# Kernel optimization log

Hardware: AMD Instinct MI355X
Metric: run time of the kernel (lower is better)

## Reference

```python
import jax, jax.numpy as jnp
import numpy as np

D_MODEL, D_STATE, D_INNER, DT_RANK, K = 64, 16, 128, 4, 4
EPS = 1e-6  # RMSNorm eps


def setup_inputs() -> dict:
    key = jax.random.key(0)
    ks = jax.random.split(key, 12)
    B, L = 8, 4096
    s = 0.02
    x = jax.random.normal(ks[0], (B, L, D_MODEL), dtype=jnp.float32)
    w_norm = jnp.ones((D_MODEL,), jnp.float32)
    W_in = jax.random.normal(ks[1], (2 * D_INNER, D_MODEL), jnp.float32) * s
    b_in = jnp.zeros((2 * D_INNER,), jnp.float32)
    W_conv = jax.random.normal(ks[2], (D_INNER, D_INNER, K), jnp.float32) * s
    b_conv = jnp.zeros((D_INNER,), jnp.float32)
    W_xp = jax.random.normal(ks[3], (DT_RANK + 2 * D_STATE, D_INNER), jnp.float32) * s
    b_xp = jnp.zeros((DT_RANK + 2 * D_STATE,), jnp.float32)
    W_dt = jax.random.normal(ks[4], (D_INNER, DT_RANK), jnp.float32) * s
    b_dt = jnp.zeros((D_INNER,), jnp.float32)
    W_out = jax.random.normal(ks[5], (D_MODEL, D_INNER), jnp.float32) * s
    b_out = jnp.zeros((D_MODEL,), jnp.float32)
    A_log = jnp.log(jnp.tile(jnp.arange(1, D_STATE + 1, dtype=jnp.float32), (D_INNER, 1)))
    D_param = jnp.ones((D_INNER,), jnp.float32)
    return dict(x=x, w_norm=w_norm, W_in=W_in, b_in=b_in, W_conv=W_conv, b_conv=b_conv,
                W_xp=W_xp, b_xp=b_xp, W_dt=W_dt, b_dt=b_dt, W_out=W_out, b_out=b_out,
                A_log=A_log, D_param=D_param)


def _mamba_block(xn, W_in, b_in, W_conv, b_conv, W_xp, b_xp, W_dt, b_dt, W_out, b_out, A_log, D_param):
    B, L, _ = xn.shape
    xz = xn @ W_in.T + b_in                      # (B,L,2*d_inner)
    u, z = jnp.split(xz, 2, axis=-1)
    z = jax.nn.silu(z)
    # conv1d: NCH, causal-style pad (K-1) both sides then truncate to L
    uc = jax.lax.conv_general_dilated(
        u.transpose(0, 2, 1), W_conv, window_strides=(1,), padding=[(K - 1, K - 1)],
        dimension_numbers=("NCH", "OIH", "NCH"))[:, :, :L] + b_conv[None, :, None]
    u = jax.nn.silu(uc.transpose(0, 2, 1))       # (B,L,d_inner)
    xp = u @ W_xp.T + b_xp
    dt, Bm, Cm = jnp.split(xp, [DT_RANK, DT_RANK + D_STATE], axis=-1)
    delta = jax.nn.softplus(dt @ W_dt.T + b_dt)  # (B,L,d_inner)
    A = -jnp.exp(A_log)                          # (d_inner, n)
    A_bar = jnp.exp(jnp.einsum('bld,dn->bldn', delta, A))
    B_bar_x = jnp.einsum('bld,bln,bld->bldn', delta, Bm, u)

    def step(h, inp):
        a, bx, c = inp                           # (B,d,n),(B,d,n),(B,n)
        h = a * h + bx
        y = jnp.einsum('bdn,bn->bd', h, c)
        return h, y

    h0 = jnp.zeros((B, D_INNER, D_STATE), xn.dtype)
    xs = (A_bar.transpose(1, 0, 2, 3), B_bar_x.transpose(1, 0, 2, 3), Cm.transpose(1, 0, 2))
    _, ys = jax.lax.scan(step, h0, xs)           # (L,B,d_inner)
    y = ys.transpose(1, 0, 2) + D_param * u
    y = y * z
    return y @ W_out.T + b_out


def reference(x, w_norm, W_in, b_in, W_conv, b_conv, W_xp, b_xp, W_dt, b_dt, W_out, b_out, A_log, D_param):
    xn = x * jax.lax.rsqrt(jnp.mean(x * x, axis=-1, keepdims=True) + EPS) * w_norm
    return x + _mamba_block(xn, W_in, b_in, W_conv, b_conv, W_xp, b_xp, W_dt, b_dt, W_out, b_out, A_log, D_param)
```

## Files before the change

### kernel.cpp

```cpp
#include <hip/hip_runtime.h>
#include <math.h>

#define D_MODEL 64
#define D_STATE 16
#define D_INNER 128
#define DT_RANK 4
#define BB 8
#define LL 4096
#define NTOK (BB*LL)
#define EPSV 1e-6f
#define NCHUNK 64
#define LC (LL/NCHUNK)
#define PAD 136
#define PADF 132

typedef __attribute__((ext_vector_type(8))) short bf16x8;
typedef __attribute__((ext_vector_type(4))) float f32x4;

__device__ __forceinline__ float sig_(float v) { return 1.f / (1.f + __expf(-v)); }
__device__ __forceinline__ float softplus_(float v) {
    return (v > 20.f) ? v : __logf(1.f + __expf(v));
}
__device__ __forceinline__ unsigned short f2bf(float x) {
    unsigned int u = __float_as_uint(x);
    u += 0x7fff + ((u >> 16) & 1);
    return (unsigned short)(u >> 16);
}
__device__ __forceinline__ float bf2f(unsigned short u) {
    return __uint_as_float(((unsigned int)u) << 16);
}

__global__ __launch_bounds__(256) void pack_all(
    const float* __restrict__ W_in, const float* __restrict__ w_norm,
    const float* __restrict__ W_conv, const float* __restrict__ W_xp,
    const float* __restrict__ W_out,
    unsigned short* __restrict__ Win_bf, unsigned short* __restrict__ Bp,
    unsigned short* __restrict__ Wxp_bf, unsigned short* __restrict__ Wout_bf)
{
    int i = blockIdx.x * 256 + threadIdx.x;
    if (i < 16384) {
        Win_bf[i] = f2bf(W_in[i] * w_norm[i & 63]);
    } else if (i < 81920) {
        int j = i - 16384;
        int kk = j >> 14, o = (j >> 7) & 127, c = j & 127;
        Bp[j] = f2bf(W_conv[o * 512 + c * 4 + kk]);
    } else if (i < 88064) {
        int j = i - 81920;
        Wxp_bf[j] = ((j >> 7) < 36) ? f2bf(W_xp[j]) : (unsigned short)0;
    } else if (i < 96256) {
        int j = i - 88064;
        Wout_bf[j] = f2bf(W_out[j]);
    }
}

__global__ __launch_bounds__(256) void k1_fused(
    const float* __restrict__ x, const unsigned short* __restrict__ Win_bf,
    const float* __restrict__ b_in,
    unsigned short* __restrict__ u_bf, unsigned short* __restrict__ z_bf)
{
    __shared__ unsigned short axs[64 * 72];
    int tid = threadIdx.x;
    int tb = blockIdx.x * 64;
    {
        int t = tid >> 2, qt = tid & 3;
        float4 v[4];
        float ss = 0.f;
        #pragma unroll
        for (int j = 0; j < 4; ++j) {
            v[j] = *(const float4*)&x[(tb + t) * 64 + qt * 16 + j * 4];
            ss += v[j].x*v[j].x + v[j].y*v[j].y + v[j].z*v[j].z + v[j].w*v[j].w;
        }
        ss += __shfl_xor(ss, 1, 64);
        ss += __shfl_xor(ss, 2, 64);
        float r = rsqrtf(ss * (1.f / 64.f) + EPSV);
        unsigned short tmp[16];
        #pragma unroll
        for (int j = 0; j < 4; ++j) {
            tmp[4*j+0] = f2bf(v[j].x * r); tmp[4*j+1] = f2bf(v[j].y * r);
            tmp[4*j+2] = f2bf(v[j].z * r); tmp[4*j+3] = f2bf(v[j].w * r);
        }
        *(bf16x8*)&axs[t * 72 + qt * 16]     = *(bf16x8*)&tmp[0];
        *(bf16x8*)&axs[t * 72 + qt * 16 + 8] = *(bf16x8*)&tmp[8];
    }
    __syncthreads();
    int wave = tid >> 6, lane = tid & 63;
    int quad = lane >> 4, l16 = lane & 15;
    f32x4 acc[16];
    #pragma unroll
    for (int nt = 0; nt < 16; ++nt) acc[nt] = (f32x4){0.f, 0.f, 0.f, 0.f};
    bf16x8 a0 = *(const bf16x8*)&axs[(wave * 16 + l16) * 72 + quad * 8];
    bf16x8 a1 = *(const bf16x8*)&axs[(wave * 16 + l16) * 72 + 32 + quad * 8];
    #pragma unroll
    for (int nt = 0; nt < 16; ++nt) {
        bf16x8 b0 = *(const bf16x8*)&Win_bf[(nt * 16 + l16) * 64 + quad * 8];
        bf16x8 b1 = *(const bf16x8*)&Win_bf[(nt * 16 + l16) * 64 + 32 + quad * 8];
        acc[nt] = __builtin_amdgcn_mfma_f32_16x16x32_bf16(a0, b0, acc[nt], 0, 0, 0);
        acc[nt] = __builtin_amdgcn_mfma_f32_16x16x32_bf16(a1, b1, acc[nt], 0, 0, 0);
    }
    #pragma unroll
    for (int nt = 0; nt < 16; ++nt) {
        int o = nt * 16 + l16;
        float bo = b_in[o];
        #pragma unroll
        for (int r = 0; r < 4; ++r) {
            int t = tb + wave * 16 + quad * 4 + r;
            float v = acc[nt][r] + bo;
            if (o < 128) u_bf[t * 128 + o] = f2bf(v);
            else         z_bf[t * 128 + (o - 128)] = f2bf(v * sig_(v));
        }
    }
}

__global__ __launch_bounds__(256) void k2k3a_fused(
    const unsigned short* __restrict__ u_bf, const unsigned short* __restrict__ Bp,
    const float* __restrict__ b_conv,
    const unsigned short* __restrict__ Wxp_bf, const float* __restrict__ b_xp,
    const float* __restrict__ W_dt, const float* __restrict__ b_dt,
    const float* __restrict__ A_log,
    unsigned short* __restrict__ u_cbf, float* __restrict__ delta,
    float* __restrict__ Bm, float* __restrict__ Cm,
    float* __restrict__ P, float* __restrict__ Q)
{
    __shared__ unsigned short uls[64 * PAD];
    __shared__ float dls[64 * PADF];
    __shared__ float bls[64 * 16];
    __shared__ float dts[64][4];
    __shared__ float Wd[512];
    __shared__ float bds[128];
    int tid = threadIdx.x;
    if (tid < 128) *(float4*)&Wd[tid * 4] = *(const float4*)&W_dt[tid * 4];
    else if (tid < 160) *(float4*)&bds[(tid - 128) * 4] = *(const float4*)&b_dt[(tid - 128) * 4];
    int wave = tid >> 6, lane = tid & 63;
    int quad = lane >> 4, l16 = lane & 15;
    int tb = blockIdx.x * 64;
    int bbase = tb & ~4095;
    int t0 = tb + wave * 16;
    f32x4 acc[8];
    #pragma unroll
    for (int og = 0; og < 8; ++og) acc[og] = (f32x4){0.f, 0.f, 0.f, 0.f};
    int row_base = t0 + l16 - 3;
    #pragma unroll
    for (int kk = 0; kk < 4; ++kk) {
        int row = row_base + kk;
        #pragma unroll
        for (int cs = 0; cs < 4; ++cs) {
            int kbase = cs * 32 + quad * 8;
            bf16x8 a = {0,0,0,0,0,0,0,0};
            if (row >= bbase)
                a = *(const bf16x8*)&u_bf[row * 128 + kbase];
            #pragma unroll
            for (int og = 0; og < 8; ++og) {
                bf16x8 b = *(const bf16x8*)&Bp[kk * 16384 + (og * 16 + l16) * 128 + kbase];
                acc[og] = __builtin_amdgcn_mfma_f32_16x16x32_bf16(a, b, acc[og], 0, 0, 0);
            }
        }
    }
    #pragma unroll
    for (int og = 0; og < 8; ++og) {
        int o = og * 16 + l16;
        float bc = b_conv[o];
        #pragma unroll
        for (int r = 0; r < 4; ++r) {
            int tloc = wave * 16 + quad * 4 + r;
            float v = acc[og][r] + bc;
            unsigned short ub = f2bf(v * sig_(v));
            u_cbf[(tb + tloc) * 128 + o] = ub;
            uls[tloc * PAD + o] = ub;
        }
    }
    __syncthreads();
    f32x4 xacc[3];
    #pragma unroll
    for (int nt = 0; nt < 3; ++nt) xacc[nt] = (f32x4){0.f, 0.f, 0.f, 0.f};
    #pragma unroll
    for (int cs = 0; cs < 4; ++cs) {
        int kbase = cs * 32 + quad * 8;
        bf16x8 a = *(const bf16x8*)&uls[(wave * 16 + l16) * PAD + kbase];
        #pragma unroll
        for (int nt = 0; nt < 3; ++nt) {
            bf16x8 b = *(const bf16x8*)&Wxp_bf[(nt * 16 + l16) * 128 + kbase];
            xacc[nt] = __builtin_amdgcn_mfma_f32_16x16x32_bf16(a, b, xacc[nt], 0, 0, 0);
        }
    }
    #pragma unroll
    for (int nt = 0; nt < 3; ++nt) {
        int j = nt * 16 + l16;
        float bx = (j < 36) ? b_xp[j] : 0.f;
        #pragma unroll
        for (int r = 0; r < 4; ++r) {
            int tloc = wave * 16 + quad * 4 + r;
            int t = tb + tloc;
            float val = xacc[nt][r] + bx;
            if (j < 4) {
                dts[tloc][j] = val;
            } else if (j < 20) {
                Bm[t * 16 + (j - 4)] = val;
                bls[tloc * 16 + (j - 4)] = val;
            } else if (j < 36) {
                Cm[t * 16 + (j - 20)] = val;
            }
        }
    }
    __syncthreads();
    {
        int tokloc = tid >> 2, dgrp = tid & 3;
        float dt0 = dts[tokloc][0], dt1 = dts[tokloc][1],
              dt2 = dts[tokloc][2], dt3 = dts[tokloc][3];
        int g = tb + tokloc;
        #pragma unroll
        for (int d4 = 0; d4 < 8; ++d4) {
            int d = dgrp * 32 + d4 * 4;
            float4 w0 = *(const float4*)&Wd[(d + 0) * 4];
            float4 w1 = *(const float4*)&Wd[(d + 1) * 4];
            float4 w2 = *(const float4*)&Wd[(d + 2) * 4];
            float4 w3 = *(const float4*)&Wd[(d + 3) * 4];
            float4 bdv = *(const float4*)&bds[d];
            float4 r;
            r.x = softplus_(bdv.x + dt0*w0.x + dt1*w0.y + dt2*w0.z + dt3*w0.w);
            r.y = softplus_(bdv.y + dt0*w1.x + dt1*w1.y + dt2*w1.z + dt3*w1.w);
            r.z = softplus_(bdv.z + dt0*w2.x + dt1*w2.y + dt2*w2.z + dt3*w2.w);
            r.w = softplus_(bdv.w + dt0*w3.x + dt1*w3.y + dt2*w3.z + dt3*w3.w);
            *(float4*)&delta[g * 128 + d] = r;
            *(float4*)&dls[tokloc * PADF + d] = r;
        }
    }
    __syncthreads();
    {
        int d = tid >> 1;
        int nb = (tid & 1) * 8;
        float4 Av0 = *(const float4*)&A_log[d * 16 + nb];
        float4 Av1 = *(const float4*)&A_log[d * 16 + nb + 4];
        float A0 = -__expf(Av0.x), A1 = -__expf(Av0.y),
              A2 = -__expf(Av0.z), A3 = -__expf(Av0.w);
        float A4 = -__expf(Av1.x), A5 = -__expf(Av1.y),
              A6 = -__expf(Av1.z), A7 = -__expf(Av1.w);
        float P0=1.f,P1=1.f,P2=1.f,P3=1.f,P4=1.f,P5=1.f,P6=1.f,P7=1.f;
        float Q0=0.f,Q1=0.f,Q2=0.f,Q3=0.f,Q4=0.f,Q5=0.f,Q6=0.f,Q7=0.f;
        for (int t = 0; t < LC; ++t) {
            float dl = dls[t * PADF + d];
            float uu = bf2f(uls[t * PAD + d]);
            float4 bm0 = *(const float4*)&bls[t * 16 + nb];
            float4 bm1 = *(const float4*)&bls[t * 16 + nb + 4];
            float du = dl * uu;
            float a0 = __expf(dl * A0), a1 = __expf(dl * A1),
                  a2 = __expf(dl * A2), a3 = __expf(dl * A3);
            float a4 = __expf(dl * A4), a5 = __expf(dl * A5),
                  a6 = __expf(dl * A6), a7 = __expf(dl * A7);
            P0 *= a0; P1 *= a1; P2 *= a2; P3 *= a3;
            P4 *= a4; P5 *= a5; P6 *= a6; P7 *= a7;
            Q0 = a0 * Q0 + du * bm0.x; Q1 = a1 * Q1 + du * bm0.y;
            Q2 = a2 * Q2 + du * bm0.z; Q3 = a3 * Q3 + du * bm0.w;
            Q4 = a4 * Q4 + du * bm1.x; Q5 = a5 * Q5 + du * bm1.y;
            Q6 = a6 * Q6 + du * bm1.z; Q7 = a7 * Q7 + du * bm1.w;
        }
        int idx = blockIdx.x * 2048 + d * 16 + nb;
        *(float4*)&P[idx]     = (float4){P0, P1, P2, P3};
        *(float4*)&P[idx + 4] = (float4){P4, P5, P6, P7};
        *(float4*)&Q[idx]     = (float4){Q0, Q1, Q2, Q3};
        *(float4*)&Q[idx + 4] = (float4){Q4, Q5, Q6, Q7};
    }
}

__global__ __launch_bounds__(256) void k4b_carry(
    const float* __restrict__ P, const float* __restrict__ Q, float* __restrict__ Hinit)
{
    int tid = blockIdx.x * 256 + threadIdx.x;
    int b = tid >> 11, dn = tid & 2047;
    float carry = 0.f;
    for (int c = 0; c < NCHUNK; ++c) {
        int idx = (b * NCHUNK + c) * 2048 + dn;
        Hinit[idx] = carry;
        carry = P[idx] * carry + Q[idx];
    }
}

__global__ __launch_bounds__(256) void k4c_scan(
    const float* __restrict__ delta, const unsigned short* __restrict__ u_cbf,
    const float* __restrict__ Bm, const float* __restrict__ Cm,
    const unsigned short* __restrict__ z_bf, const float* __restrict__ A_log,
    const float* __restrict__ D_param, const float* __restrict__ Hinit,
    unsigned short* __restrict__ y_bf)
{
    __shared__ float dls[LC * 64];
    __shared__ unsigned short uls[LC * 64];
    __shared__ float bls[LC * 16];
    __shared__ float cls[LC * 16];
    __shared__ unsigned short zls[LC * 64];
    int bid = blockIdx.x;
    int b = bid >> 7, c = (bid >> 1) & 63, half = bid & 1;
    int tid = threadIdx.x, lane = tid & 63;
    int g0 = b * LL + c * LC;
    int d0 = half * 64;
    for (int i = tid; i < LC * 16; i += 256) {
        int row = i >> 4, q = i & 15;
        *(float4*)&dls[row * 64 + q * 4] =
            *(const float4*)&delta[(g0 + row) * 128 + d0 + q * 4];
    }
    for (int i = tid; i < LC * 8; i += 256) {
        int row = i >> 3, q = i & 7;
        *(float4*)&uls[row * 64 + q * 8] =
            *(const float4*)&u_cbf[(g0 + row) * 128 + d0 + q * 8];
        *(float4*)&zls[row * 64 + q * 8] =
            *(const float4*)&z_bf[(g0 + row) * 128 + d0 + q * 8];
    }
    for (int i = tid; i < LC * 4; i += 256) {
        int row = i >> 2, q = i & 3;
        *(float4*)&bls[row * 16 + q * 4] =
            *(const float4*)&Bm[(g0 + row) * 16 + q * 4];
        *(float4*)&cls[row * 16 + q * 4] =
            *(const float4*)&Cm[(g0 + row) * 16 + q * 4];
    }
    int dloc = (tid >> 6) * 16 + (lane >> 2);
    int d = d0 + dloc;
    int ng = lane & 3;
    float4 Av = *(const float4*)&A_log[d * 16 + ng * 4];
    float A0 = -__expf(Av.x), A1 = -__expf(Av.y), A2 = -__expf(Av.z), A3 = -__expf(Av.w);
    float4 h = *(const float4*)&Hinit[(b * NCHUNK + c) * 2048 + d * 16 + ng * 4];
    float Dp = D_param[d];
    __syncthreads();
    for (int t = 0; t < LC; ++t) {
        float dl = dls[t * 64 + dloc];
        float uu = bf2f(uls[t * 64 + dloc]);
        float4 bm = *(const float4*)&bls[t * 16 + ng * 4];
        float4 cm = *(const float4*)&cls[t * 16 + ng * 4];
        float du = dl * uu;
        float a0 = __expf(dl * A0), a1 = __expf(dl * A1),
              a2 = __expf(dl * A2), a3 = __expf(dl * A3);
        h.x = a0 * h.x + du * bm.x; h.y = a1 * h.y + du * bm.y;
        h.z = a2 * h.z + du * bm.z; h.w = a3 * h.w + du * bm.w;
        float yv = h.x * cm.x + h.y * cm.y + h.z * cm.z + h.w * cm.w;
        yv += __shfl_xor(yv, 1, 64);
        yv += __shfl_xor(yv, 2, 64);
        if (ng == 0) {
            float y = yv + Dp * uu;
            y *= bf2f(zls[t * 64 + dloc]);
            y_bf[(g0 + t) * 128 + d] = f2bf(y);
        }
    }
}

__global__ __launch_bounds__(256) void k5_outproj_mfma(
    const unsigned short* __restrict__ y_bf, const unsigned short* __restrict__ Wout_bf,
    const float* __restrict__ b_out, const float* __restrict__ x,
    float* __restrict__ out)
{
    int tid = threadIdx.x;
    int wave = tid >> 6, lane = tid & 63;
    int quad = lane >> 4, l16 = lane & 15;
    int t0 = blockIdx.x * 64 + wave * 16;
    f32x4 acc[4];
    #pragma unroll
    for (int nt = 0; nt < 4; ++nt) acc[nt] = (f32x4){0.f, 0.f, 0.f, 0.f};
    #pragma unroll
    for (int cs = 0; cs < 4; ++cs) {
        int kbase = cs * 32 + quad * 8;
        bf16x8 a = *(const bf16x8*)&y_bf[(t0 + l16) * 128 + kbase];
        #pragma unroll
        for (int nt = 0; nt < 4; ++nt) {
            bf16x8 b = *(const bf16x8*)&Wout_bf[(nt * 16 + l16) * 128 + kbase];
            acc[nt] = __builtin_amdgcn_mfma_f32_16x16x32_bf16(a, b, acc[nt], 0, 0, 0);
        }
    }
    #pragma unroll
    for (int nt = 0; nt < 4; ++nt) {
        int m = nt * 16 + l16;
        float bo = b_out[m];
        #pragma unroll
        for (int r = 0; r < 4; ++r) {
            int t = t0 + quad * 4 + r;
            out[t * 64 + m] = acc[nt][r] + bo + x[t * 64 + m];
        }
    }
}

extern "C" void kernel_launch(void* const* d_in, const int* in_sizes, int n_in,
                              void* d_out, int out_size, void* d_ws, size_t ws_size,
                              hipStream_t stream)
{
    const float* x       = (const float*)d_in[0];
    const float* w_norm  = (const float*)d_in[1];
    const float* W_in    = (const float*)d_in[2];
    const float* b_in    = (const float*)d_in[3];
    const float* W_conv  = (const float*)d_in[4];
    const float* b_conv  = (const float*)d_in[5];
    const float* W_xp    = (const float*)d_in[6];
    const float* b_xp    = (const float*)d_in[7];
    const float* W_dt    = (const float*)d_in[8];
    const float* b_dt    = (const float*)d_in[9];
    const float* W_out   = (const float*)d_in[10];
    const float* b_out   = (const float*)d_in[11];
    const float* A_log   = (const float*)d_in[12];
    const float* D_param = (const float*)d_in[13];
    float* ws = (float*)d_ws;

    unsigned short* u_bf = (unsigned short*)ws;
    unsigned short* y_bf = (unsigned short*)ws;
    unsigned short* z_bf = (unsigned short*)(ws + 2097152);
    unsigned short* u_cbf= (unsigned short*)(ws + 4194304);
    float* delta  = ws + 6291456;
    float* Bm     = ws + 10485760;
    float* Cm     = ws + 11010048;
    float* P      = ws + 11534336;
    float* Q      = ws + 12582912;
    float* Hinit  = ws + 13631488;
    unsigned short* Bp      = (unsigned short*)(ws + 14680064);
    unsigned short* Wxp_bf  = (unsigned short*)(ws + 14712832);
    unsigned short* Wout_bf = (unsigned short*)(ws + 14715904);
    unsigned short* Win_bf  = (unsigned short*)(ws + 14720000);
    float* out    = (float*)d_out;

    pack_all<<<376, 256, 0, stream>>>(W_in, w_norm, W_conv, W_xp, W_out,
                                      Win_bf, Bp, Wxp_bf, Wout_bf);
    k1_fused<<<512, 256, 0, stream>>>(x, Win_bf, b_in, u_bf, z_bf);
    k2k3a_fused<<<512, 256, 0, stream>>>(u_bf, Bp, b_conv, Wxp_bf, b_xp,
                                         W_dt, b_dt, A_log,
                                         u_cbf, delta, Bm, Cm, P, Q);
    k4b_carry<<<64, 256, 0, stream>>>(P, Q, Hinit);
    k4c_scan<<<1024, 256, 0, stream>>>(delta, u_cbf, Bm, Cm, z_bf, A_log,
                                       D_param, Hinit, y_bf);
    k5_outproj_mfma<<<512, 256, 0, stream>>>(y_bf, Wout_bf, b_out, x, out);
}
```

Before: 196.9 us.

## Fuse chunked scan with output projection, keeping y in shared memory

Merges the per-chunk selective scan and the MFMA output projection into one kernel. Each block now handles a full 64-token chunk across all 128 channels, writes gated y into padded LDS and runs the out-projection from there, so the y_bf global round trip and one launch go away. Each thread now owns 8 states instead of 4, which halves the shuffle reduction but cuts the block count to 512. Delta is also stored in LDS as bf16 rather than fp32, which lowers precision in the exp and update math.

```diff
diff --git a/kernel.cpp b/kernel.cpp
--- a/kernel.cpp
+++ b/kernel.cpp
@@ -28,6 +28,9 @@
 }
 __device__ __forceinline__ float bf2f(unsigned short u) {
     return __uint_as_float(((unsigned int)u) << 16);
+}
+__device__ __forceinline__ unsigned int pack2bf(float a, float b) {
+    return (unsigned int)f2bf(a) | ((unsigned int)f2bf(b) << 16);
 }
 
 __global__ __launch_bounds__(256) void pack_all(
@@ -274,91 +277,90 @@
     }
 }
 
-__global__ __launch_bounds__(256) void k4c_scan(
+__global__ __launch_bounds__(256) void k4c5_fused(
     const float* __restrict__ delta, const unsigned short* __restrict__ u_cbf,
     const float* __restrict__ Bm, const float* __restrict__ Cm,
     const unsigned short* __restrict__ z_bf, const float* __restrict__ A_log,
     const float* __restrict__ D_param, const float* __restrict__ Hinit,
-    unsigned short* __restrict__ y_bf)
-{
-    __shared__ float dls[LC * 64];
-    __shared__ unsigned short uls[LC * 64];
+    const unsigned short* __restrict__ Wout_bf, const float* __restrict__ b_out,
+    const float* __restrict__ x, float* __restrict__ out)
+{
+    __shared__ unsigned short dls[LC * 128];
+    __shared__ unsigned short uls[LC * 128];
     __shared__ float bls[LC * 16];
     __shared__ float cls[LC * 16];
-    __shared__ unsigned short zls[LC * 64];
+    __shared__ unsigned short yzls[LC * PAD];
     int bid = blockIdx.x;
-    int b = bid >> 7, c = (bid >> 1) & 63, half = bid & 1;
     int tid = threadIdx.x, lane = tid & 63;
-    int g0 = b * LL + c * LC;
-    int d0 = half * 64;
+    int g0 = bid * 64;
+    for (int i = tid; i < LC * 32; i += 256) {
+        int row = i >> 5, q = i & 31;
+        float4 v = *(const float4*)&delta[(g0 + row) * 128 + q * 4];
+        uint2 pk; pk.x = pack2bf(v.x, v.y); pk.y = pack2bf(v.z, v.w);
+        *(uint2*)&dls[row * 128 + q * 4] = pk;
+    }
     for (int i = tid; i < LC * 16; i += 256) {
         int row = i >> 4, q = i & 15;
-        *(float4*)&dls[row * 64 + q * 4] =
-            *(const float4*)&delta[(g0 + row) * 128 + d0 + q * 4];
-    }
-    for (int i = tid; i < LC * 8; i += 256) {
-        int row = i >> 3, q = i & 7;
-        *(float4*)&uls[row * 64 + q * 8] =
-            *(const float4*)&u_cbf[(g0 + row) * 128 + d0 + q * 8];
-        *(float4*)&zls[row * 64 + q * 8] =
-            *(const float4*)&z_bf[(g0 + row) * 128 + d0 + q * 8];
+        *(float4*)&uls[row * 128 + q * 8] =
+            *(const float4*)&u_cbf[(g0 + row) * 128 + q * 8];
+        *(float4*)&yzls[row * PAD + q * 8] =
+            *(const float4*)&z_bf[(g0 + row) * 128 + q * 8];
     }
     for (int i = tid; i < LC * 4; i += 256) {
         int row = i >> 2, q = i & 3;
-        *(float4*)&bls[row * 16 + q * 4] =
-            *(const float4*)&Bm[(g0 + row) * 16 + q * 4];
-        *(float4*)&cls[row * 16 + q * 4] =
-            *(const float4*)&Cm[(g0 + row) * 16 + q * 4];
-    }
-    int dloc = (tid >> 6) * 16 + (lane >> 2);
-    int d = d0 + dloc;
-    int ng = lane & 3;
-    float4 Av = *(const float4*)&A_log[d * 16 + ng * 4];
-    float A0 = -__expf(Av.x), A1 = -__expf(Av.y), A2 = -__expf(Av.z), A3 = -__expf(Av.w);
-    float4 h = *(const float4*)&Hinit[(b * NCHUNK + c) * 2048 + d * 16 + ng * 4];
+        *(float4*)&bls[row * 16 + q * 4] = *(const float4*)&Bm[(g0 + row) * 16 + q * 4];
+        *(float4*)&cls[row * 16 + q * 4] = *(const float4*)&Cm[(g0 + row) * 16 + q * 4];
+    }
+    int d = tid >> 1;
+    int nb = (tid & 1) * 8;
+    float4 Av0 = *(const float4*)&A_log[d * 16 + nb];
+    float4 Av1 = *(const float4*)&A_log[d * 16 + nb + 4];
+    float A0 = -__expf(Av0.x), A1 = -__expf(Av0.y), A2 = -__expf(Av0.z), A3 = -__expf(Av0.w);
+    float A4 = -__expf(Av1.x), A5 = -__expf(Av1.y), A6 = -__expf(Av1.z), A7 = -__expf(Av1.w);
+    int hbase = bid * 2048 + d * 16 + nb;
+    float4 h0 = *(const float4*)&Hinit[hbase];
+    float4 h1 = *(const float4*)&Hinit[hbase + 4];
     float Dp = D_param[d];
     __syncthreads();
     for (int t = 0; t < LC; ++t) {
-        float dl = dls[t * 64 + dloc];
-        float uu = bf2f(uls[t * 64 + dloc]);
-        float4 bm = *(const float4*)&bls[t * 16 + ng * 4];
-        float4 cm = *(const float4*)&cls[t * 16 + ng * 4];
+        float dl = bf2f(dls[t * 128 + d]);
+        float uu = bf2f(uls[t * 128 + d]);
+        float4 bm0 = *(const float4*)&bls[t * 16 + nb];
+        float4 bm1 = *(const float4*)&bls[t * 16 + nb + 4];
+        float4 cm0 = *(const float4*)&cls[t * 16 + nb];
+        float4 cm1 = *(const float4*)&cls[t * 16 + nb + 4];
         float du = dl * uu;
         float a0 = __expf(dl * A0), a1 = __expf(dl * A1),
               a2 = __expf(dl * A2), a3 = __expf(dl * A3);
-        h.x = a0 * h.x + du * bm.x; h.y = a1 * h.y + du * bm.y;
-        h.z = a2 * h.z + du * bm.z; h.w = a3 * h.w + du * bm.w;
-        float yv = h.x * cm.x + h.y * cm.y + h.z * cm.z + h.w * cm.w;
+        float a4 = __expf(dl * A4), a5 = __expf(dl * A5),
+              a6 = __expf(dl * A6), a7 = __expf(dl * A7);
+        h0.x = a0 * h0.x + du * bm0.x; h0.y = a1 * h0.y + du * bm0.y;
+        h0.z = a2 * h0.z + du * bm0.z; h0.w = a3 * h0.w + du * bm0.w;
+        h1.x = a4 * h1.x + du * bm1.x; h1.y = a5 * h1.y + du * bm1.y;
+        h1.z = a6 * h1.z + du * bm1.z; h1.w = a7 * h1.w + du * bm1.w;
+        float yv = h0.x * cm0.x + h0.y * cm0.y + h0.z * cm0.z + h0.w * cm0.w
+                 + h1.x * cm1.x + h1.y * cm1.y + h1.z * cm1.z + h1.w * cm1.w;
         yv += __shfl_xor(yv, 1, 64);
-        yv += __shfl_xor(yv, 2, 64);
-        if (ng == 0) {
+        if ((tid & 1) == 0) {
             float y = yv + Dp * uu;
-            y *= bf2f(zls[t * 64 + dloc]);
-            y_bf[(g0 + t) * 128 + d] = f2bf(y);
-        }
-    }
-}
-
-__global__ __launch_bounds__(256) void k5_outproj_mfma(
-    const unsigned short* __restrict__ y_bf, const unsigned short* __restrict__ Wout_bf,
-    const float* __restrict__ b_out, const float* __restrict__ x,
-    float* __restrict__ out)
-{
-    int tid = threadIdx.x;
-    int wave = tid >> 6, lane = tid & 63;
+            y *= bf2f(yzls[t * PAD + d]);
+            yzls[t * PAD + d] = f2bf(y);
+        }
+    }
+    __syncthreads();
+    int wave = tid >> 6;
     int quad = lane >> 4, l16 = lane & 15;
-    int t0 = blockIdx.x * 64 + wave * 16;
-    f32x4 acc[4];
-    #pragma unroll
-    for (int nt = 0; nt < 4; ++nt) acc[nt] = (f32x4){0.f, 0.f, 0.f, 0.f};
+    f32x4 oacc[4];
+    #pragma unroll
+    for (int nt = 0; nt < 4; ++nt) oacc[nt] = (f32x4){0.f, 0.f, 0.f, 0.f};
     #pragma unroll
     for (int cs = 0; cs < 4; ++cs) {
         int kbase = cs * 32 + quad * 8;
-        bf16x8 a = *(const bf16x8*)&y_bf[(t0 + l16) * 128 + kbase];
+        bf16x8 a = *(const bf16x8*)&yzls[(wave * 16 + l16) * PAD + kbase];
         #pragma unroll
         for (int nt = 0; nt < 4; ++nt) {
-            bf16x8 b = *(const bf16x8*)&Wout_bf[(nt * 16 + l16) * 128 + kbase];
-            acc[nt] = __builtin_amdgcn_mfma_f32_16x16x32_bf16(a, b, acc[nt], 0, 0, 0);
+            bf16x8 bb = *(const bf16x8*)&Wout_bf[(nt * 16 + l16) * 128 + kbase];
+            oacc[nt] = __builtin_amdgcn_mfma_f32_16x16x32_bf16(a, bb, oacc[nt], 0, 0, 0);
         }
     }
     #pragma unroll
@@ -367,8 +369,8 @@
         float bo = b_out[m];
         #pragma unroll
         for (int r = 0; r < 4; ++r) {
-            int t = t0 + quad * 4 + r;
-            out[t * 64 + m] = acc[nt][r] + bo + x[t * 64 + m];
+            int t = g0 + wave * 16 + quad * 4 + r;
+            out[t * 64 + m] = oacc[nt][r] + bo + x[t * 64 + m];
         }
     }
 }
@@ -394,7 +396,6 @@
     float* ws = (float*)d_ws;
 
     unsigned short* u_bf = (unsigned short*)ws;
-    unsigned short* y_bf = (unsigned short*)ws;
     unsigned short* z_bf = (unsigned short*)(ws + 2097152);
     unsigned short* u_cbf= (unsigned short*)(ws + 4194304);
     float* delta  = ws + 6291456;
@@ -416,7 +417,6 @@
                                          W_dt, b_dt, A_log,
                                          u_cbf, delta, Bm, Cm, P, Q);
     k4b_carry<<<64, 256, 0, stream>>>(P, Q, Hinit);
-    k4c_scan<<<1024, 256, 0, stream>>>(delta, u_cbf, Bm, Cm, z_bf, A_log,
-                                       D_param, Hinit, y_bf);
-    k5_outproj_mfma<<<512, 256, 0, stream>>>(y_bf, Wout_bf, b_out, x, out);
-}
+    k4c5_fused<<<512, 256, 0, stream>>>(delta, u_cbf, Bm, Cm, z_bf, A_log,
+                                        D_param, Hinit, Wout_bf, b_out, x, out);
+}
```

After: 188.9 us. 4.1% less time.
